# Kernel optimization log

Measured on AMD Instinct MI355X. Metric: run time of the kernel, lower is better.

## Reference

```python
import jax, jax.numpy as jnp
import numpy as np

D_MODEL = 512
NHEAD = 8
D_HEAD = D_MODEL // NHEAD
SCALE = D_HEAD ** -0.5
EPS = 1e-8


def setup_inputs() -> dict:
    key = jax.random.key(0)
    ks = jax.random.split(key, 12)
    B, N = 4, 2048
    s = D_MODEL ** -0.5
    return {
        "Q_input": jax.random.normal(ks[0], (B, N, D_MODEL), jnp.float32),
        "KV_input": jax.random.normal(ks[1], (B, N, D_MODEL), jnp.float32),
        "SC": jax.random.uniform(ks[2], (B, N, N), jnp.float32),
        "Wq_w": jax.random.normal(ks[3], (D_MODEL, D_MODEL), jnp.float32) * s,
        "Wq_b": jnp.zeros((D_MODEL,), jnp.float32),
        "Wk_w": jax.random.normal(ks[4], (D_MODEL, D_MODEL), jnp.float32) * s,
        "Wk_b": jnp.zeros((D_MODEL,), jnp.float32),
        "Wv_w": jax.random.normal(ks[5], (D_MODEL, D_MODEL), jnp.float32) * s,
        "Wv_b": jnp.zeros((D_MODEL,), jnp.float32),
        "gate_w": jax.random.normal(ks[6], (), jnp.float32),
        "gate_b": jnp.zeros((), jnp.float32),
        "out_w": jax.random.normal(ks[7], (D_MODEL, D_MODEL), jnp.float32) * s,
        "out_b": jnp.zeros((D_MODEL,), jnp.float32),
    }


def reference(Q_input, KV_input, SC, Wq_w, Wq_b, Wk_w, Wk_b, Wv_w, Wv_b,
              gate_w, gate_b, out_w, out_b):
    B, N, _ = Q_input.shape
    # projections -> [B, H, N, d_head]
    def proj(x, w, b):
        y = x @ w.T + b
        return y.reshape(B, N, NHEAD, D_HEAD).transpose(0, 2, 1, 3)
    Q = proj(Q_input, Wq_w, Wq_b)
    K = proj(KV_input, Wk_w, Wk_b)
    V = proj(KV_input, Wv_w, Wv_b)
    # scores [B, H, N, N]
    scores = jnp.einsum('bhqd,bhkd->bhqk', Q, K) * SCALE
    # per-edge gate: sigmoid(w*SC + b), broadcast over heads
    g = jax.nn.sigmoid(SC * gate_w + gate_b)  # [B, N, N]
    scores = scores + jnp.log(g + EPS)[:, None, :, :]
    attn = jax.nn.softmax(scores, axis=-1)
    out = jnp.einsum('bhqk,bhkd->bhqd', attn, V)
    out = out.transpose(0, 2, 1, 3).reshape(B, N, D_MODEL)
    return out @ out_w.T + out_b
```

## Files before the change

### kernel.cpp

```cpp
#include <hip/hip_runtime.h>

typedef unsigned short u16;
typedef unsigned int u32;
typedef __attribute__((ext_vector_type(4))) float f32x4;
typedef __attribute__((ext_vector_type(8))) short s16x8;
typedef __attribute__((ext_vector_type(4))) u16 u16x4;
typedef __attribute__((ext_vector_type(2))) u32 u32x2;

#define L2E 1.4426950408889634f
#define QSCALE 0.18033688011112042f

__device__ __forceinline__ u16 f2bf(float f) {
    union { float f; u32 i; } v; v.f = f;
    return (u16)((v.i + 0x7fffu + ((v.i >> 16) & 1u)) >> 16);
}
__device__ __forceinline__ u32 pack_hi(float a, float b) {
    union { float f; u32 i; } x, y; x.f = a; y.f = b;
    return __builtin_amdgcn_perm(y.i, x.i, 0x07060302u);
}
__device__ __forceinline__ float bflo(u32 w) {
    union { u32 i; float f; } v; v.i = w << 16; return v.f;
}
__device__ __forceinline__ float bfhi(u32 w) {
    union { u32 i; float f; } v; v.i = w & 0xFFFF0000u; return v.f;
}

__device__ __forceinline__ void gl2lds16(const u16* g, u16* l) {
    __builtin_amdgcn_global_load_lds(
        (const __attribute__((address_space(1))) void*)g,
        (__attribute__((address_space(3))) void*)l, 16, 0, 0);
}

__global__ __launch_bounds__(256) void conv_kernel(
    const float* __restrict__ s0, const float* __restrict__ s1,
    const float* __restrict__ s2, const float* __restrict__ s3,
    const float* __restrict__ s4, const float* __restrict__ s5,
    u16* __restrict__ dst)
{
    int e = (blockIdx.x * 256 + threadIdx.x) * 4;
    const float* src; int off;
    if      (e < 4194304) { src = s0; off = e; }
    else if (e < 8388608) { src = s1; off = e - 4194304; }
    else if (e < 8650752) { src = s2; off = e - 8388608; }
    else if (e < 8912896) { src = s3; off = e - 8650752; }
    else if (e < 9175040) { src = s4; off = e - 8912896; }
    else                  { src = s5; off = e - 9175040; }
    f32x4 f = *(const f32x4*)(src + off);
    u16x4 o;
#pragma unroll
    for (int j = 0; j < 4; ++j) o[j] = f2bf(f[j]);
    *(u16x4*)(dst + e) = o;
}

__device__ __forceinline__ void gemm_core(
    const u16* __restrict__ A, const u16* __restrict__ Bw,
    int m0, int n0, u16* As, u16* Bs, f32x4 acc[4][4])
{
    const int tid = threadIdx.x;
    const int lane = tid & 63, w = tid >> 6;
    const int wm = w >> 1, wn = w & 1;
    const int l16 = lane & 15, quad = lane >> 4;
    const int srow = (lane >> 2), sch = (lane & 3) * 8;
    const f32x4 vzero = {0.f, 0.f, 0.f, 0.f};
#pragma unroll
    for (int i = 0; i < 4; ++i)
#pragma unroll
        for (int j = 0; j < 4; ++j) acc[i][j] = vzero;

#pragma unroll
    for (int j = 0; j < 2; ++j) {
        int row = w * 32 + j * 16 + srow;
        gl2lds16(&A[(size_t)(m0 + row) * 512 + sch], &As[w * 1024 + j * 512]);
        gl2lds16(&Bw[(size_t)(n0 + row) * 512 + sch], &Bs[w * 1024 + j * 512]);
    }
    for (int kt = 0; kt < 16; ++kt) {
        __syncthreads();
        const int cur = (kt & 1) * 4096;
        if (kt < 15) {
            const int nxt = ((kt + 1) & 1) * 4096;
#pragma unroll
            for (int j = 0; j < 2; ++j) {
                int row = w * 32 + j * 16 + srow;
                gl2lds16(&A[(size_t)(m0 + row) * 512 + (kt + 1) * 32 + sch],
                         &As[nxt + w * 1024 + j * 512]);
                gl2lds16(&Bw[(size_t)(n0 + row) * 512 + (kt + 1) * 32 + sch],
                         &Bs[nxt + w * 1024 + j * 512]);
            }
        }
        s16x8 af[4], bfr[4];
#pragma unroll
        for (int mt = 0; mt < 4; ++mt)
            af[mt] = *(const s16x8*)&As[cur + (wm * 64 + mt * 16 + l16) * 32 + quad * 8];
#pragma unroll
        for (int nt = 0; nt < 4; ++nt)
            bfr[nt] = *(const s16x8*)&Bs[cur + (wn * 64 + nt * 16 + l16) * 32 + quad * 8];
#pragma unroll
        for (int mt = 0; mt < 4; ++mt)
#pragma unroll
            for (int nt = 0; nt < 4; ++nt)
                acc[mt][nt] = __builtin_amdgcn_mfma_f32_16x16x32_bf16(
                    af[mt], bfr[nt], acc[mt][nt], 0, 0, 0);
    }
}

__device__ __forceinline__ void gemm_core_m64(
    const u16* __restrict__ A, const u16* __restrict__ Bw,
    int m0, int n0, u16* As, u16* Bs, f32x4 acc[2][4])
{
    const int tid = threadIdx.x;
    const int lane = tid & 63, w = tid >> 6;
    const int wm = w & 1, wn = w >> 1;
    const int l16 = lane & 15, quad = lane >> 4;
    const int srow = (lane >> 2), sch = (lane & 3) * 8;
    const f32x4 vzero = {0.f, 0.f, 0.f, 0.f};
#pragma unroll
    for (int i = 0; i < 2; ++i)
#pragma unroll
        for (int j = 0; j < 4; ++j) acc[i][j] = vzero;

    gl2lds16(&A[(size_t)(m0 + w * 16 + srow) * 512 + sch], &As[w * 512]);
#pragma unroll
    for (int j = 0; j < 2; ++j) {
        int row = w * 32 + j * 16 + srow;
        gl2lds16(&Bw[(size_t)(n0 + row) * 512 + sch], &Bs[w * 1024 + j * 512]);
    }
    for (int kt = 0; kt < 16; ++kt) {
        __syncthreads();
        const int curA = (kt & 1) * 2048, curB = (kt & 1) * 4096;
        if (kt < 15) {
            const int nxtA = ((kt + 1) & 1) * 2048, nxtB = ((kt + 1) & 1) * 4096;
            gl2lds16(&A[(size_t)(m0 + w * 16 + srow) * 512 + (kt + 1) * 32 + sch],
                     &As[nxtA + w * 512]);
#pragma unroll
            for (int j = 0; j < 2; ++j) {
                int row = w * 32 + j * 16 + srow;
                gl2lds16(&Bw[(size_t)(n0 + row) * 512 + (kt + 1) * 32 + sch],
                         &Bs[nxtB + w * 1024 + j * 512]);
            }
        }
        s16x8 af[2], bfr[4];
#pragma unroll
        for (int mt = 0; mt < 2; ++mt)
            af[mt] = *(const s16x8*)&As[curA + (wm * 32 + mt * 16 + l16) * 32 + quad * 8];
#pragma unroll
        for (int nt = 0; nt < 4; ++nt)
            bfr[nt] = *(const s16x8*)&Bs[curB + (wn * 64 + nt * 16 + l16) * 32 + quad * 8];
#pragma unroll
        for (int mt = 0; mt < 2; ++mt)
#pragma unroll
            for (int nt = 0; nt < 4; ++nt)
                acc[mt][nt] = __builtin_amdgcn_mfma_f32_16x16x32_bf16(
                    af[mt], bfr[nt], acc[mt][nt], 0, 0, 0);
    }
}

__global__ __launch_bounds__(256) void projlg_kernel(
    const u16* __restrict__ cQin, const u16* __restrict__ cKV,
    const u16* __restrict__ cW,
    const float* __restrict__ bq, const float* __restrict__ bk,
    const float* __restrict__ bv,
    u16* __restrict__ Qh, u16* __restrict__ Kh, u16* __restrict__ Vt,
    const float* __restrict__ SC, const float* __restrict__ gwp,
    const float* __restrict__ gbp, u16* __restrict__ LGx)
{
    __shared__ __align__(16) u16 As[2 * 4096];
    __shared__ __align__(16) u16 Bs[2 * 4096];
    if (blockIdx.x < 768) {
        const int job = blockIdx.x >> 8;
        const int rem = blockIdx.x & 255;
        const int n0 = (rem & 3) * 128, m0 = (rem >> 2) * 128;
        const u16* A = (job == 0) ? cQin : cKV;
        const u16* W = cW + (size_t)job * 262144;
        const float* bias = (job == 0) ? bq : (job == 1 ? bk : bv);
        f32x4 acc[4][4];
        gemm_core(A, W, m0, n0, As, Bs, acc);

        const int tid = threadIdx.x, lane = tid & 63, w = tid >> 6;
        const int wm = w >> 1, wn = w & 1, l16 = lane & 15, quad = lane >> 4;
#pragma unroll
        for (int nt = 0; nt < 4; ++nt) {
            int j = n0 + wn * 64 + nt * 16 + l16;
            float bj = bias[j];
            int h = j >> 6, d = j & 63;
#pragma unroll
            for (int mt = 0; mt < 4; ++mt) {
                int trow = m0 + wm * 64 + mt * 16 + quad * 4;
                int bb = trow >> 11, nn = trow & 2047;
                int bh = bb * 8 + h;
                if (job == 2) {
                    u16x4 pv;
#pragma unroll
                    for (int reg = 0; reg < 4; ++reg) pv[reg] = f2bf(acc[mt][nt][reg] + bj);
                    *(u16x4*)&Vt[(size_t)(bh * 64 + d) * 2048 + nn] = pv;
                } else if (job == 0) {
#pragma unroll
                    for (int reg = 0; reg < 4; ++reg)
                        Qh[(size_t)(bh * 2048 + nn + reg) * 64 + d] =
                            f2bf((acc[mt][nt][reg] + bj) * QSCALE);
                } else {
#pragma unroll
                    for (int reg = 0; reg < 4; ++reg)
                        Kh[(size_t)(bh * 2048 + nn + reg) * 64 + d] =
                            f2bf(acc[mt][nt][reg] + bj);
                }
            }
        }
    } else {
        const int flat = (blockIdx.x - 768) * 256 + threadIdx.x;
        const int lane = flat & 63;
        const int kt   = (flat >> 6) & 31;
        const int t16  = (flat >> 11) & 127;
        const int b    = flat >> 18;
        const int l16 = lane & 15, quad = lane >> 4;
        const float tA = -gwp[0] * L2E, tB = -gbp[0] * L2E;
        const float* row = SC + ((size_t)b * 2048 + t16 * 16 + l16) * 2048
                              + kt * 64 + quad * 4;
        __align__(16) u16 tmp[16];
#pragma unroll
        for (int kk = 0; kk < 4; ++kk) {
            f32x4 x = *(const f32x4*)(row + kk * 16);
#pragma unroll
            for (int reg = 0; reg < 4; ++reg) {
                float g = __builtin_amdgcn_rcpf(
                    1.0f + __builtin_amdgcn_exp2f(tA * x[reg] + tB)) + 1e-8f;
                tmp[kk * 4 + reg] = f2bf(__builtin_amdgcn_logf(g));
            }
        }
        u16* d = LGx + (size_t)flat * 16;
        *(uint4*)d       = *(uint4*)tmp;
        *(uint4*)(d + 8) = *(uint4*)(tmp + 8);
    }
}

__global__ __launch_bounds__(256, 2) void attn_kernel(
    const u16* __restrict__ Qh, const u16* __restrict__ Kh,
    const u16* __restrict__ Vt, const u16* __restrict__ LGx,
    u16* __restrict__ Ob)
{
    __shared__ __align__(16) u16 Ks[2][8192];
    __shared__ __align__(16) u16 Vs[2][8192];
    const int tid = threadIdx.x;
    const int w = tid >> 6, lane = tid & 63;
    const int l16 = lane & 15, quad = lane >> 4;
    const int b = blockIdx.z, head = blockIdx.y, qg = blockIdx.x;
    const int bh = b * 8 + head;
    const int q0a = qg * 128 + w * 32, q0b = q0a + 16;
    const int t16a = qg * 8 + w * 2;
    const u16* Qp = Qh + (size_t)bh * 131072;
    const u16* Kp = Kh + (size_t)bh * 131072;
    const u16* Vp = Vt + (size_t)bh * 131072;
    const u16* lgPa = LGx + ((size_t)((b * 128 + t16a) * 32) * 64 + lane) * 16;
    const u16* lgPb = LGx + ((size_t)((b * 128 + t16a + 1) * 32) * 64 + lane) * 16;
    const f32x4 vzero = {0.f, 0.f, 0.f, 0.f};
    const s16x8 ones = {0x3F80, 0x3F80, 0x3F80, 0x3F80,
                        0x3F80, 0x3F80, 0x3F80, 0x3F80};

    const int s3 = l16 & 7, s2x = s3 & 3, s4x = s3 & 4;
    const int qsw = (quad ^ s2x) * 8;
    const int rb0 = l16 * 64 + qsw + s4x * 8;
    const int rb1 = l16 * 64 + qsw + (4 ^ s4x) * 8;
    const u16* KbL = &Ks[0][0];
    const u16* VbL = &Vs[0][0];

    const int sr = lane >> 3, c8 = lane & 7;
    const bool isK = (w < 2);
    const int hv = w & 1;
    const u16* sgq = isK
        ? (Kp + (size_t)(hv * 64 + sr) * 64 + (c8 ^ sr) * 8)
        : (Vp + (size_t)sr * 2048 + hv * 64 + (c8 ^ sr) * 8);
    const size_t slabAdv = isK ? 512 : 16384;
    const size_t tileAdv = isK ? 8192 : 128;
    u16* sdb = isK ? &Ks[0][hv * 4096] : &Vs[0][hv * 4096];

    s16x8 qfa0 = *(const s16x8*)&Qp[(size_t)(q0a + l16) * 64 + quad * 8];
    s16x8 qfa1 = *(const s16x8*)&Qp[(size_t)(q0a + l16) * 64 + 32 + quad * 8];
    s16x8 qfb0 = *(const s16x8*)&Qp[(size_t)(q0b + l16) * 64 + quad * 8];
    s16x8 qfb1 = *(const s16x8*)&Qp[(size_t)(q0b + l16) * 64 + 32 + quad * 8];
    f32x4 oA[4], oB[4], laccA = vzero, laccB = vzero;
#pragma unroll
    for (int dn = 0; dn < 4; ++dn) { oA[dn] = vzero; oB[dn] = vzero; }

#pragma unroll
    for (int j = 0; j < 8; ++j)
        gl2lds16(sgq + (size_t)j * slabAdv, sdb + j * 512);
    sgq += tileAdv;
    uint4 lga0 = *(const uint4*)lgPa;
    uint4 lga1 = *(const uint4*)(lgPa + 8);
    uint4 lga2 = *(const uint4*)(lgPa + 1024);
    uint4 lga3 = *(const uint4*)(lgPa + 1032);
    uint4 lgb0 = *(const uint4*)lgPb;
    uint4 lgb1 = *(const uint4*)(lgPb + 8);
    uint4 lgb2 = *(const uint4*)(lgPb + 1024);
    uint4 lgb3 = *(const uint4*)(lgPb + 1032);
    lgPa += 2048; lgPb += 2048;

#define QKQUAD(LA, LB, MA, MB, KOFF)                                           \
    {                                                                          \
        const u32 wda[8] = {LA.x, LA.y, LA.z, LA.w, LB.x, LB.y, LB.z, LB.w};   \
        const u32 wdb[8] = {MA.x, MA.y, MA.z, MA.w, MB.x, MB.y, MB.z, MB.w};   \
        _Pragma("unroll")                                                      \
        for (int kk = 0; kk < 4; ++kk) {                                       \
            s16x8 ka = *(const s16x8*)(KbL + bo + rb0 + kk * 1024);            \
            s16x8 kb = *(const s16x8*)(KbL + bo + rb1 + kk * 1024);            \
            f32x4 ci;                                                          \
            ci[0] = bflo(wda[kk * 2]);     ci[1] = bfhi(wda[kk * 2]);          \
            ci[2] = bflo(wda[kk * 2 + 1]); ci[3] = bfhi(wda[kk * 2 + 1]);      \
            f32x4 s = __builtin_amdgcn_mfma_f32_16x16x32_bf16(ka, qfa0, ci, 0, 0, 0); \
            s = __builtin_amdgcn_mfma_f32_16x16x32_bf16(kb, qfa1, s, 0, 0, 0); \
            f32x4 cj;                                                          \
            cj[0] = bflo(wdb[kk * 2]);     cj[1] = bfhi(wdb[kk * 2]);          \
            cj[2] = bflo(wdb[kk * 2 + 1]); cj[3] = bfhi(wdb[kk * 2 + 1]);      \
            f32x4 t = __builtin_amdgcn_mfma_f32_16x16x32_bf16(ka, qfb0, cj, 0, 0, 0); \
            t = __builtin_amdgcn_mfma_f32_16x16x32_bf16(kb, qfb1, t, 0, 0, 0); \
            PwA[kk][0] = pack_hi(__builtin_amdgcn_exp2f(s[0]),                 \
                                 __builtin_amdgcn_exp2f(s[1]));                \
            PwA[kk][1] = pack_hi(__builtin_amdgcn_exp2f(s[2]),                 \
                                 __builtin_amdgcn_exp2f(s[3]));                \
            PwB[kk][0] = pack_hi(__builtin_amdgcn_exp2f(t[0]),                 \
                                 __builtin_amdgcn_exp2f(t[1]));                \
            PwB[kk][1] = pack_hi(__builtin_amdgcn_exp2f(t[2]),                 \
                                 __builtin_amdgcn_exp2f(t[3]));                \
        }                                                                      \
    }

    for (int kt = 0; kt < 16; ++kt) {
        __syncthreads();
        const int bo = (kt & 1) * 8192;
        if (kt < 15) {
            u16* dd = sdb + (8192 - bo);
#pragma unroll
            for (int j = 0; j < 8; ++j)
                gl2lds16(sgq + (size_t)j * slabAdv, dd + j * 512);
            sgq += tileAdv;
        }
        __builtin_amdgcn_s_setprio(1);
        u32 PwA8[8][2], PwB8[8][2];
        {
            u32 (*PwA)[2] = &PwA8[0];
            u32 (*PwB)[2] = &PwB8[0];
            QKQUAD(lga0, lga1, lgb0, lgb1, 0);
        }
        {
            const int bo2 = bo + 4096;
            u32 (*PwA)[2] = &PwA8[4];
            u32 (*PwB)[2] = &PwB8[4];
            const int bo_save = bo2 - 4096;
            {
                const u32 wda[8] = {lga2.x, lga2.y, lga2.z, lga2.w,
                                    lga3.x, lga3.y, lga3.z, lga3.w};
                const u32 wdb[8] = {lgb2.x, lgb2.y, lgb2.z, lgb2.w,
                                    lgb3.x, lgb3.y, lgb3.z, lgb3.w};
#pragma unroll
                for (int kk = 0; kk < 4; ++kk) {
                    s16x8 ka = *(const s16x8*)(KbL + bo_save + rb0 + (4 + kk) * 1024);
                    s16x8 kb = *(const s16x8*)(KbL + bo_save + rb1 + (4 + kk) * 1024);
                    f32x4 ci;
                    ci[0] = bflo(wda[kk * 2]);     ci[1] = bfhi(wda[kk * 2]);
                    ci[2] = bflo(wda[kk * 2 + 1]); ci[3] = bfhi(wda[kk * 2 + 1]);
                    f32x4 s = __builtin_amdgcn_mfma_f32_16x16x32_bf16(ka, qfa0, ci, 0, 0, 0);
                    s = __builtin_amdgcn_mfma_f32_16x16x32_bf16(kb, qfa1, s, 0, 0, 0);
                    f32x4 cj;
                    cj[0] = bflo(wdb[kk * 2]);     cj[1] = bfhi(wdb[kk * 2]);
                    cj[2] = bflo(wdb[kk * 2 + 1]); cj[3] = bfhi(wdb[kk * 2 + 1]);
                    f32x4 t = __builtin_amdgcn_mfma_f32_16x16x32_bf16(ka, qfb0, cj, 0, 0, 0);
                    t = __builtin_amdgcn_mfma_f32_16x16x32_bf16(kb, qfb1, t, 0, 0, 0);
                    PwA[kk][0] = pack_hi(__builtin_amdgcn_exp2f(s[0]),
                                         __builtin_amdgcn_exp2f(s[1]));
                    PwA[kk][1] = pack_hi(__builtin_amdgcn_exp2f(s[2]),
                                         __builtin_amdgcn_exp2f(s[3]));
                    PwB[kk][0] = pack_hi(__builtin_amdgcn_exp2f(t[0]),
                                         __builtin_amdgcn_exp2f(t[1]));
                    PwB[kk][1] = pack_hi(__builtin_amdgcn_exp2f(t[2]),
                                         __builtin_amdgcn_exp2f(t[3]));
                }
            }
        }
        if (kt < 15) {
            lga0 = *(const uint4*)lgPa;
            lga1 = *(const uint4*)(lgPa + 8);
            lga2 = *(const uint4*)(lgPa + 1024);
            lga3 = *(const uint4*)(lgPa + 1032);
            lgb0 = *(const uint4*)lgPb;
            lgb1 = *(const uint4*)(lgPb + 8);
            lgb2 = *(const uint4*)(lgPb + 1024);
            lgb3 = *(const uint4*)(lgPb + 1032);
            lgPa += 2048; lgPb += 2048;
        }
#pragma unroll
        for (int kc = 0; kc < 4; ++kc) {
            union { u32 wrd[4]; s16x8 v; } pa, pb;
#pragma unroll
            for (int i = 0; i < 2; ++i) {
                u32x2 r1 = __builtin_amdgcn_permlane32_swap(
                    PwA8[2 * kc][i], PwA8[2 * kc + 1][i], false, false);
                u32x2 r2 = __builtin_amdgcn_permlane16_swap(
                    r1[0], r1[1], false, false);
                pa.wrd[i]     = r2[0];
                pa.wrd[2 + i] = r2[1];
                u32x2 r3 = __builtin_amdgcn_permlane32_swap(
                    PwB8[2 * kc][i], PwB8[2 * kc + 1][i], false, false);
                u32x2 r4 = __builtin_amdgcn_permlane16_swap(
                    r3[0], r3[1], false, false);
                pb.wrd[i]     = r4[0];
                pb.wrd[2 + i] = r4[1];
            }
            s16x8 pfa = pa.v, pfb = pb.v;
            laccA = __builtin_amdgcn_mfma_f32_16x16x32_bf16(pfa, ones, laccA, 0, 0, 0);
            laccB = __builtin_amdgcn_mfma_f32_16x16x32_bf16(pfb, ones, laccB, 0, 0, 0);
            const int vbb = ((kc & 1) ? rb1 : rb0) + (kc >> 1) * 4096 + bo;
#pragma unroll
            for (int dn = 0; dn < 4; ++dn) {
                s16x8 vf = *(const s16x8*)(VbL + vbb + dn * 1024);
                oA[dn] = __builtin_amdgcn_mfma_f32_16x16x32_bf16(
                    pfa, vf, oA[dn], 0, 0, 0);
                oB[dn] = __builtin_amdgcn_mfma_f32_16x16x32_bf16(
                    pfb, vf, oB[dn], 0, 0, 0);
            }
        }
        __builtin_amdgcn_s_setprio(0);
    }
#undef QKQUAD
#pragma unroll
    for (int reg = 0; reg < 4; ++reg) {
        float invA = __builtin_amdgcn_rcpf(laccA[reg]);
        float invB = __builtin_amdgcn_rcpf(laccB[reg]);
        int trowA = b * 2048 + q0a + quad * 4 + reg;
        int trowB = b * 2048 + q0b + quad * 4 + reg;
#pragma unroll
        for (int dn = 0; dn < 4; ++dn) {
            Ob[(size_t)trowA * 512 + head * 64 + dn * 16 + l16] =
                f2bf(oA[dn][reg] * invA);
            Ob[(size_t)trowB * 512 + head * 64 + dn * 16 + l16] =
                f2bf(oB[dn][reg] * invB);
        }
    }
}

__global__ __launch_bounds__(256) void out_kernel(
    const u16* __restrict__ Ob, const u16* __restrict__ cWo,
    const float* __restrict__ bo, float* __restrict__ out)
{
    __shared__ __align__(16) u16 As[2 * 2048];
    __shared__ __align__(16) u16 Bs[2 * 4096];
    const int m0 = blockIdx.y * 64, n0 = blockIdx.x * 128;
    f32x4 acc[2][4];
    gemm_core_m64(Ob, cWo, m0, n0, As, Bs, acc);
    const int tid = threadIdx.x, lane = tid & 63, w = tid >> 6;
    const int wm = w & 1, wn = w >> 1, l16 = lane & 15, quad = lane >> 4;
#pragma unroll
    for (int nt = 0; nt < 4; ++nt) {
        int j = n0 + wn * 64 + nt * 16 + l16;
        float bj = bo[j];
#pragma unroll
        for (int mt = 0; mt < 2; ++mt) {
            int t = m0 + wm * 32 + mt * 16 + quad * 4;
#pragma unroll
            for (int reg = 0; reg < 4; ++reg)
                out[(size_t)(t + reg) * 512 + j] = acc[mt][nt][reg] + bj;
        }
    }
}

extern "C" void kernel_launch(void* const* d_in, const int* in_sizes, int n_in,
                              void* d_out, int out_size, void* d_ws, size_t ws_size,
                              hipStream_t stream)
{
    const float* Qin  = (const float*)d_in[0];
    const float* KVin = (const float*)d_in[1];
    const float* SC   = (const float*)d_in[2];
    const float* Wq   = (const float*)d_in[3];
    const float* bq   = (const float*)d_in[4];
    const float* Wk   = (const float*)d_in[5];
    const float* bk   = (const float*)d_in[6];
    const float* Wv   = (const float*)d_in[7];
    const float* bv   = (const float*)d_in[8];
    const float* gw   = (const float*)d_in[9];
    const float* gb   = (const float*)d_in[10];
    const float* Wo   = (const float*)d_in[11];
    const float* bo   = (const float*)d_in[12];
    float* out = (float*)d_out;

    u16* conv = (u16*)d_ws;
    u16* cQin = conv;
    u16* cKV  = conv + 4194304;
    u16* cW   = conv + 8388608;
    u16* Qh   = conv + 9437184;
    u16* Kh   = Qh + 4194304;
    u16* Vt   = Kh + 4194304;
    u16* Ob   = Vt + 4194304;
    u16* LGx  = Ob + 4194304;

    hipLaunchKernelGGL(conv_kernel, dim3(9216), dim3(256), 0, stream,
                       Qin, KVin, Wq, Wk, Wv, Wo, conv);
    hipLaunchKernelGGL(projlg_kernel, dim3(4864), dim3(256), 0, stream,
                       cQin, cKV, cW, bq, bk, bv, Qh, Kh, Vt,
                       SC, gw, gb, LGx);
    hipLaunchKernelGGL(attn_kernel, dim3(16, 8, 4), dim3(256), 0, stream,
                       Qh, Kh, Vt, LGx, Ob);
    hipLaunchKernelGGL(out_kernel, dim3(4, 128), dim3(256), 0, stream,
                       Ob, cW + 786432, bo, out);
}
```

Baseline: 235.9 us.

## Fuse fp32-to-bf16 conversion into GEMM loads and drop LDS staging

Removes the separate conversion kernel and has the projection and output GEMMs read fp32 inputs and weights straight from global memory. Each fragment is converted in registers with packed bf16 convert instructions. LDS double-buffering and the block barriers in both GEMMs are dropped, so each wave loads its own fragments directly. This saves a launch and a full bf16 copy of the activations and weights. In exchange, operands are read twice as wide, there is no cross-wave reuse through shared memory, and global loads are strided with no prefetch, which may leave the MFMA units waiting on memory.

```diff
diff --git a/kernel.cpp b/kernel.cpp
--- a/kernel.cpp
+++ b/kernel.cpp
@@ -24,6 +24,21 @@
 __device__ __forceinline__ float bfhi(u32 w) {
     union { u32 i; float f; } v; v.i = w & 0xFFFF0000u; return v.f;
 }
+__device__ __forceinline__ u32 cvtpk_bf16(float a, float b) {
+    u32 d;
+    asm("v_cvt_pk_bf16_f32 %0, %1, %2" : "=v"(d) : "v"(a), "v"(b));
+    return d;
+}
+__device__ __forceinline__ s16x8 ldfrag_f32(const float* __restrict__ p) {
+    f32x4 x = *(const f32x4*)p;
+    f32x4 y = *(const f32x4*)(p + 4);
+    union { u32 w[4]; s16x8 v; } u;
+    u.w[0] = cvtpk_bf16(x[0], x[1]);
+    u.w[1] = cvtpk_bf16(x[2], x[3]);
+    u.w[2] = cvtpk_bf16(y[0], y[1]);
+    u.w[3] = cvtpk_bf16(y[2], y[3]);
+    return u.v;
+}
 
 __device__ __forceinline__ void gl2lds16(const u16* g, u16* l) {
     __builtin_amdgcn_global_load_lds(
@@ -31,69 +46,30 @@
         (__attribute__((address_space(3))) void*)l, 16, 0, 0);
 }
 
-__global__ __launch_bounds__(256) void conv_kernel(
-    const float* __restrict__ s0, const float* __restrict__ s1,
-    const float* __restrict__ s2, const float* __restrict__ s3,
-    const float* __restrict__ s4, const float* __restrict__ s5,
-    u16* __restrict__ dst)
-{
-    int e = (blockIdx.x * 256 + threadIdx.x) * 4;
-    const float* src; int off;
-    if      (e < 4194304) { src = s0; off = e; }
-    else if (e < 8388608) { src = s1; off = e - 4194304; }
-    else if (e < 8650752) { src = s2; off = e - 8388608; }
-    else if (e < 8912896) { src = s3; off = e - 8650752; }
-    else if (e < 9175040) { src = s4; off = e - 8912896; }
-    else                  { src = s5; off = e - 9175040; }
-    f32x4 f = *(const f32x4*)(src + off);
-    u16x4 o;
-#pragma unroll
-    for (int j = 0; j < 4; ++j) o[j] = f2bf(f[j]);
-    *(u16x4*)(dst + e) = o;
-}
-
-__device__ __forceinline__ void gemm_core(
-    const u16* __restrict__ A, const u16* __restrict__ Bw,
-    int m0, int n0, u16* As, u16* Bs, f32x4 acc[4][4])
+__device__ __forceinline__ void gemm_f32_nolds(
+    const float* __restrict__ A, const float* __restrict__ Bw,
+    int m0, int n0, f32x4 acc[4][4])
 {
     const int tid = threadIdx.x;
     const int lane = tid & 63, w = tid >> 6;
     const int wm = w >> 1, wn = w & 1;
     const int l16 = lane & 15, quad = lane >> 4;
-    const int srow = (lane >> 2), sch = (lane & 3) * 8;
     const f32x4 vzero = {0.f, 0.f, 0.f, 0.f};
 #pragma unroll
     for (int i = 0; i < 4; ++i)
 #pragma unroll
         for (int j = 0; j < 4; ++j) acc[i][j] = vzero;
 
-#pragma unroll
-    for (int j = 0; j < 2; ++j) {
-        int row = w * 32 + j * 16 + srow;
-        gl2lds16(&A[(size_t)(m0 + row) * 512 + sch], &As[w * 1024 + j * 512]);
-        gl2lds16(&Bw[(size_t)(n0 + row) * 512 + sch], &Bs[w * 1024 + j * 512]);
-    }
+    const float* ap0 = A + (size_t)(m0 + wm * 64 + l16) * 512 + quad * 8;
+    const float* bp0 = Bw + (size_t)(n0 + wn * 64 + l16) * 512 + quad * 8;
     for (int kt = 0; kt < 16; ++kt) {
-        __syncthreads();
-        const int cur = (kt & 1) * 4096;
-        if (kt < 15) {
-            const int nxt = ((kt + 1) & 1) * 4096;
-#pragma unroll
-            for (int j = 0; j < 2; ++j) {
-                int row = w * 32 + j * 16 + srow;
-                gl2lds16(&A[(size_t)(m0 + row) * 512 + (kt + 1) * 32 + sch],
-                         &As[nxt + w * 1024 + j * 512]);
-                gl2lds16(&Bw[(size_t)(n0 + row) * 512 + (kt + 1) * 32 + sch],
-                         &Bs[nxt + w * 1024 + j * 512]);
-            }
-        }
         s16x8 af[4], bfr[4];
 #pragma unroll
         for (int mt = 0; mt < 4; ++mt)
-            af[mt] = *(const s16x8*)&As[cur + (wm * 64 + mt * 16 + l16) * 32 + quad * 8];
+            af[mt] = ldfrag_f32(ap0 + (size_t)mt * 16 * 512 + kt * 32);
 #pragma unroll
         for (int nt = 0; nt < 4; ++nt)
-            bfr[nt] = *(const s16x8*)&Bs[cur + (wn * 64 + nt * 16 + l16) * 32 + quad * 8];
+            bfr[nt] = ldfrag_f32(bp0 + (size_t)nt * 16 * 512 + kt * 32);
 #pragma unroll
         for (int mt = 0; mt < 4; ++mt)
 #pragma unroll
@@ -103,48 +79,30 @@
     }
 }
 
-__device__ __forceinline__ void gemm_core_m64(
-    const u16* __restrict__ A, const u16* __restrict__ Bw,
-    int m0, int n0, u16* As, u16* Bs, f32x4 acc[2][4])
+__device__ __forceinline__ void gemm_m64_nolds(
+    const u16* __restrict__ A, const float* __restrict__ Bw,
+    int m0, int n0, f32x4 acc[2][4])
 {
     const int tid = threadIdx.x;
     const int lane = tid & 63, w = tid >> 6;
     const int wm = w & 1, wn = w >> 1;
     const int l16 = lane & 15, quad = lane >> 4;
-    const int srow = (lane >> 2), sch = (lane & 3) * 8;
     const f32x4 vzero = {0.f, 0.f, 0.f, 0.f};
 #pragma unroll
     for (int i = 0; i < 2; ++i)
 #pragma unroll
         for (int j = 0; j < 4; ++j) acc[i][j] = vzero;
 
-    gl2lds16(&A[(size_t)(m0 + w * 16 + srow) * 512 + sch], &As[w * 512]);
-#pragma unroll
-    for (int j = 0; j < 2; ++j) {
-        int row = w * 32 + j * 16 + srow;
-        gl2lds16(&Bw[(size_t)(n0 + row) * 512 + sch], &Bs[w * 1024 + j * 512]);
-    }
+    const u16* ap0 = A + (size_t)(m0 + wm * 32 + l16) * 512 + quad * 8;
+    const float* bp0 = Bw + (size_t)(n0 + wn * 64 + l16) * 512 + quad * 8;
     for (int kt = 0; kt < 16; ++kt) {
-        __syncthreads();
-        const int curA = (kt & 1) * 2048, curB = (kt & 1) * 4096;
-        if (kt < 15) {
-            const int nxtA = ((kt + 1) & 1) * 2048, nxtB = ((kt + 1) & 1) * 4096;
-            gl2lds16(&A[(size_t)(m0 + w * 16 + srow) * 512 + (kt + 1) * 32 + sch],
-                     &As[nxtA + w * 512]);
-#pragma unroll
-            for (int j = 0; j < 2; ++j) {
-                int row = w * 32 + j * 16 + srow;
-                gl2lds16(&Bw[(size_t)(n0 + row) * 512 + (kt + 1) * 32 + sch],
-                         &Bs[nxtB + w * 1024 + j * 512]);
-            }
-        }
         s16x8 af[2], bfr[4];
 #pragma unroll
         for (int mt = 0; mt < 2; ++mt)
-            af[mt] = *(const s16x8*)&As[curA + (wm * 32 + mt * 16 + l16) * 32 + quad * 8];
+            af[mt] = *(const s16x8*)(ap0 + (size_t)mt * 16 * 512 + kt * 32);
 #pragma unroll
         for (int nt = 0; nt < 4; ++nt)
-            bfr[nt] = *(const s16x8*)&Bs[curB + (wn * 64 + nt * 16 + l16) * 32 + quad * 8];
+            bfr[nt] = ldfrag_f32(bp0 + (size_t)nt * 16 * 512 + kt * 32);
 #pragma unroll
         for (int mt = 0; mt < 2; ++mt)
 #pragma unroll
@@ -155,25 +113,24 @@
 }
 
 __global__ __launch_bounds__(256) void projlg_kernel(
-    const u16* __restrict__ cQin, const u16* __restrict__ cKV,
-    const u16* __restrict__ cW,
+    const float* __restrict__ Qin, const float* __restrict__ KVin,
+    const float* __restrict__ Wq, const float* __restrict__ Wk,
+    const float* __restrict__ Wv,
     const float* __restrict__ bq, const float* __restrict__ bk,
     const float* __restrict__ bv,
     u16* __restrict__ Qh, u16* __restrict__ Kh, u16* __restrict__ Vt,
     const float* __restrict__ SC, const float* __restrict__ gwp,
     const float* __restrict__ gbp, u16* __restrict__ LGx)
 {
-    __shared__ __align__(16) u16 As[2 * 4096];
-    __shared__ __align__(16) u16 Bs[2 * 4096];
     if (blockIdx.x < 768) {
         const int job = blockIdx.x >> 8;
         const int rem = blockIdx.x & 255;
         const int n0 = (rem & 3) * 128, m0 = (rem >> 2) * 128;
-        const u16* A = (job == 0) ? cQin : cKV;
-        const u16* W = cW + (size_t)job * 262144;
+        const float* A = (job == 0) ? Qin : KVin;
+        const float* W = (job == 0) ? Wq : (job == 1 ? Wk : Wv);
         const float* bias = (job == 0) ? bq : (job == 1 ? bk : bv);
         f32x4 acc[4][4];
-        gemm_core(A, W, m0, n0, As, Bs, acc);
+        gemm_f32_nolds(A, W, m0, n0, acc);
 
         const int tid = threadIdx.x, lane = tid & 63, w = tid >> 6;
         const int wm = w >> 1, wn = w & 1, l16 = lane & 15, quad = lane >> 4;
@@ -294,35 +251,6 @@
     uint4 lgb3 = *(const uint4*)(lgPb + 1032);
     lgPa += 2048; lgPb += 2048;
 
-#define QKQUAD(LA, LB, MA, MB, KOFF)                                           \
-    {                                                                          \
-        const u32 wda[8] = {LA.x, LA.y, LA.z, LA.w, LB.x, LB.y, LB.z, LB.w};   \
-        const u32 wdb[8] = {MA.x, MA.y, MA.z, MA.w, MB.x, MB.y, MB.z, MB.w};   \
-        _Pragma("unroll")                                                      \
-        for (int kk = 0; kk < 4; ++kk) {                                       \
-            s16x8 ka = *(const s16x8*)(KbL + bo + rb0 + kk * 1024);            \
-            s16x8 kb = *(const s16x8*)(KbL + bo + rb1 + kk * 1024);            \
-            f32x4 ci;                                                          \
-            ci[0] = bflo(wda[kk * 2]);     ci[1] = bfhi(wda[kk * 2]);          \
-            ci[2] = bflo(wda[kk * 2 + 1]); ci[3] = bfhi(wda[kk * 2 + 1]);      \
-            f32x4 s = __builtin_amdgcn_mfma_f32_16x16x32_bf16(ka, qfa0, ci, 0, 0, 0); \
-            s = __builtin_amdgcn_mfma_f32_16x16x32_bf16(kb, qfa1, s, 0, 0, 0); \
-            f32x4 cj;                                                          \
-            cj[0] = bflo(wdb[kk * 2]);     cj[1] = bfhi(wdb[kk * 2]);          \
-            cj[2] = bflo(wdb[kk * 2 + 1]); cj[3] = bfhi(wdb[kk * 2 + 1]);      \
-            f32x4 t = __builtin_amdgcn_mfma_f32_16x16x32_bf16(ka, qfb0, cj, 0, 0, 0); \
-            t = __builtin_amdgcn_mfma_f32_16x16x32_bf16(kb, qfb1, t, 0, 0, 0); \
-            PwA[kk][0] = pack_hi(__builtin_amdgcn_exp2f(s[0]),                 \
-                                 __builtin_amdgcn_exp2f(s[1]));                \
-            PwA[kk][1] = pack_hi(__builtin_amdgcn_exp2f(s[2]),                 \
-                                 __builtin_amdgcn_exp2f(s[3]));                \
-            PwB[kk][0] = pack_hi(__builtin_amdgcn_exp2f(t[0]),                 \
-                                 __builtin_amdgcn_exp2f(t[1]));                \
-            PwB[kk][1] = pack_hi(__builtin_amdgcn_exp2f(t[2]),                 \
-                                 __builtin_amdgcn_exp2f(t[3]));                \
-        }                                                                      \
-    }
-
     for (int kt = 0; kt < 16; ++kt) {
         __syncthreads();
         const int bo = (kt & 1) * 8192;
@@ -336,43 +264,61 @@
         __builtin_amdgcn_s_setprio(1);
         u32 PwA8[8][2], PwB8[8][2];
         {
-            u32 (*PwA)[2] = &PwA8[0];
-            u32 (*PwB)[2] = &PwB8[0];
-            QKQUAD(lga0, lga1, lgb0, lgb1, 0);
+            const u32 wda[8] = {lga0.x, lga0.y, lga0.z, lga0.w,
+                                lga1.x, lga1.y, lga1.z, lga1.w};
+            const u32 wdb[8] = {lgb0.x, lgb0.y, lgb0.z, lgb0.w,
+                                lgb1.x, lgb1.y, lgb1.z, lgb1.w};
+#pragma unroll
+            for (int kk = 0; kk < 4; ++kk) {
+                s16x8 ka = *(const s16x8*)(KbL + bo + rb0 + kk * 1024);
+                s16x8 kb = *(const s16x8*)(KbL + bo + rb1 + kk * 1024);
+                f32x4 ci;
+                ci[0] = bflo(wda[kk * 2]);     ci[1] = bfhi(wda[kk * 2]);
+                ci[2] = bflo(wda[kk * 2 + 1]); ci[3] = bfhi(wda[kk * 2 + 1]);
+                f32x4 s = __builtin_amdgcn_mfma_f32_16x16x32_bf16(ka, qfa0, ci, 0, 0, 0);
+                s = __builtin_amdgcn_mfma_f32_16x16x32_bf16(kb, qfa1, s, 0, 0, 0);
+                f32x4 cj;
+                cj[0] = bflo(wdb[kk * 2]);     cj[1] = bfhi(wdb[kk * 2]);
+                cj[2] = bflo(wdb[kk * 2 + 1]); cj[3] = bfhi(wdb[kk * 2 + 1]);
+                f32x4 t = __builtin_amdgcn_mfma_f32_16x16x32_bf16(ka, qfb0, cj, 0, 0, 0);
+                t = __builtin_amdgcn_mfma_f32_16x16x32_bf16(kb, qfb1, t, 0, 0, 0);
+                PwA8[kk][0] = pack_hi(__builtin_amdgcn_exp2f(s[0]),
+                                      __builtin_amdgcn_exp2f(s[1]));
+                PwA8[kk][1] = pack_hi(__builtin_amdgcn_exp2f(s[2]),
+                                      __builtin_amdgcn_exp2f(s[3]));
+                PwB8[kk][0] = pack_hi(__builtin_amdgcn_exp2f(t[0]),
+                                      __builtin_amdgcn_exp2f(t[1]));
+                PwB8[kk][1] = pack_hi(__builtin_amdgcn_exp2f(t[2]),
+                                      __builtin_amdgcn_exp2f(t[3]));
+            }
         }
         {
-            const int bo2 = bo + 4096;
-            u32 (*PwA)[2] = &PwA8[4];
-            u32 (*PwB)[2] = &PwB8[4];
-            const int bo_save = bo2 - 4096;
-            {
-                const u32 wda[8] = {lga2.x, lga2.y, lga2.z, lga2.w,
-                                    lga3.x, lga3.y, lga3.z, lga3.w};
-                const u32 wdb[8] = {lgb2.x, lgb2.y, lgb2.z, lgb2.w,
-                                    lgb3.x, lgb3.y, lgb3.z, lgb3.w};
-#pragma unroll
-                for (int kk = 0; kk < 4; ++kk) {
-                    s16x8 ka = *(const s16x8*)(KbL + bo_save + rb0 + (4 + kk) * 1024);
-                    s16x8 kb = *(const s16x8*)(KbL + bo_save + rb1 + (4 + kk) * 1024);
-                    f32x4 ci;
-                    ci[0] = bflo(wda[kk * 2]);     ci[1] = bfhi(wda[kk * 2]);
-                    ci[2] = bflo(wda[kk * 2 + 1]); ci[3] = bfhi(wda[kk * 2 + 1]);
-                    f32x4 s = __builtin_amdgcn_mfma_f32_16x16x32_bf16(ka, qfa0, ci, 0, 0, 0);
-                    s = __builtin_amdgcn_mfma_f32_16x16x32_bf16(kb, qfa1, s, 0, 0, 0);
-                    f32x4 cj;
-                    cj[0] = bflo(wdb[kk * 2]);     cj[1] = bfhi(wdb[kk * 2]);
-                    cj[2] = bflo(wdb[kk * 2 + 1]); cj[3] = bfhi(wdb[kk * 2 + 1]);
-                    f32x4 t = __builtin_amdgcn_mfma_f32_16x16x32_bf16(ka, qfb0, cj, 0, 0, 0);
-                    t = __builtin_amdgcn_mfma_f32_16x16x32_bf16(kb, qfb1, t, 0, 0, 0);
-                    PwA[kk][0] = pack_hi(__builtin_amdgcn_exp2f(s[0]),
-                                         __builtin_amdgcn_exp2f(s[1]));
-                    PwA[kk][1] = pack_hi(__builtin_amdgcn_exp2f(s[2]),
-                                         __builtin_amdgcn_exp2f(s[3]));
-                    PwB[kk][0] = pack_hi(__builtin_amdgcn_exp2f(t[0]),
-                                         __builtin_amdgcn_exp2f(t[1]));
-                    PwB[kk][1] = pack_hi(__builtin_amdgcn_exp2f(t[2]),
-                                         __builtin_amdgcn_exp2f(t[3]));
-                }
+            const u32 wda[8] = {lga2.x, lga2.y, lga2.z, lga2.w,
+                                lga3.x, lga3.y, lga3.z, lga3.w};
+            const u32 wdb[8] = {lgb2.x, lgb2.y, lgb2.z, lgb2.w,
+                                lgb3.x, lgb3.y, lgb3.z, lgb3.w};
+#pragma unroll
+            for (int kk = 0; kk < 4; ++kk) {
+                s16x8 ka = *(const s16x8*)(KbL + bo + rb0 + (4 + kk) * 1024);
+                s16x8 kb = *(const s16x8*)(KbL + bo + rb1 + (4 + kk) * 1024);
+                f32x4 ci;
+                ci[0] = bflo(wda[kk * 2]);     ci[1] = bfhi(wda[kk * 2]);
+                ci[2] = bflo(wda[kk * 2 + 1]); ci[3] = bfhi(wda[kk * 2 + 1]);
+                f32x4 s = __builtin_amdgcn_mfma_f32_16x16x32_bf16(ka, qfa0, ci, 0, 0, 0);
+                s = __builtin_amdgcn_mfma_f32_16x16x32_bf16(kb, qfa1, s, 0, 0, 0);
+                f32x4 cj;
+                cj[0] = bflo(wdb[kk * 2]);     cj[1] = bfhi(wdb[kk * 2]);
+                cj[2] = bflo(wdb[kk * 2 + 1]); cj[3] = bfhi(wdb[kk * 2 + 1]);
+                f32x4 t = __builtin_amdgcn_mfma_f32_16x16x32_bf16(ka, qfb0, cj, 0, 0, 0);
+                t = __builtin_amdgcn_mfma_f32_16x16x32_bf16(kb, qfb1, t, 0, 0, 0);
+                PwA8[4 + kk][0] = pack_hi(__builtin_amdgcn_exp2f(s[0]),
+                                          __builtin_amdgcn_exp2f(s[1]));
+                PwA8[4 + kk][1] = pack_hi(__builtin_amdgcn_exp2f(s[2]),
+                                          __builtin_amdgcn_exp2f(s[3]));
+                PwB8[4 + kk][0] = pack_hi(__builtin_amdgcn_exp2f(t[0]),
+                                          __builtin_amdgcn_exp2f(t[1]));
+                PwB8[4 + kk][1] = pack_hi(__builtin_amdgcn_exp2f(t[2]),
+                                          __builtin_amdgcn_exp2f(t[3]));
             }
         }
         if (kt < 15) {
@@ -419,7 +365,6 @@
         }
         __builtin_amdgcn_s_setprio(0);
     }
-#undef QKQUAD
 #pragma unroll
     for (int reg = 0; reg < 4; ++reg) {
         float invA = __builtin_amdgcn_rcpf(laccA[reg]);
@@ -437,14 +382,12 @@
 }
 
 __global__ __launch_bounds__(256) void out_kernel(
-    const u16* __restrict__ Ob, const u16* __restrict__ cWo,
+    const u16* __restrict__ Ob, const float* __restrict__ Wo,
     const float* __restrict__ bo, float* __restrict__ out)
 {
-    __shared__ __align__(16) u16 As[2 * 2048];
-    __shared__ __align__(16) u16 Bs[2 * 4096];
     const int m0 = blockIdx.y * 64, n0 = blockIdx.x * 128;
     f32x4 acc[2][4];
-    gemm_core_m64(Ob, cWo, m0, n0, As, Bs, acc);
+    gemm_m64_nolds(Ob, Wo, m0, n0, acc);
     const int tid = threadIdx.x, lane = tid & 63, w = tid >> 6;
     const int wm = w & 1, wn = w >> 1, l16 = lane & 15, quad = lane >> 4;
 #pragma unroll
@@ -480,23 +423,17 @@
     const float* bo   = (const float*)d_in[12];
     float* out = (float*)d_out;
 
-    u16* conv = (u16*)d_ws;
-    u16* cQin = conv;
-    u16* cKV  = conv + 4194304;
-    u16* cW   = conv + 8388608;
-    u16* Qh   = conv + 9437184;
+    u16* Qh   = (u16*)d_ws;
     u16* Kh   = Qh + 4194304;
     u16* Vt   = Kh + 4194304;
     u16* Ob   = Vt + 4194304;
     u16* LGx  = Ob + 4194304;
 
-    hipLaunchKernelGGL(conv_kernel, dim3(9216), dim3(256), 0, stream,
-                       Qin, KVin, Wq, Wk, Wv, Wo, conv);
     hipLaunchKernelGGL(projlg_kernel, dim3(4864), dim3(256), 0, stream,
-                       cQin, cKV, cW, bq, bk, bv, Qh, Kh, Vt,
+                       Qin, KVin, Wq, Wk, Wv, bq, bk, bv, Qh, Kh, Vt,
                        SC, gw, gb, LGx);
     hipLaunchKernelGGL(attn_kernel, dim3(16, 8, 4), dim3(256), 0, stream,
                        Qh, Kh, Vt, LGx, Ob);
     hipLaunchKernelGGL(out_kernel, dim3(4, 128), dim3(256), 0, stream,
-                       Ob, cW + 786432, bo, out);
-}
+                       Ob, Wo, bo, out);
+}
```

After: 320.8 us. 36.0% more time.
